# Kernel optimization log

Hardware: AMD Instinct MI355X
Metric: run time of the kernel (lower is better)

## Reference

```python
import jax, jax.numpy as jnp
import numpy as np

H = 16          # num heads
D = 128         # head dim
WIN = 128       # local sliding window
EPS = 1e-6
ROPE_BASE = 500000.0


def rmsnorm(x, w, eps=EPS):
    var = jnp.mean(x * x, axis=-1, keepdims=True)
    return x * jax.lax.rsqrt(var + eps) * w


def rope(x, positions):
    # x: [T, H, D], neox-style rotate-halves
    half = D // 2
    inv_freq = 1.0 / (ROPE_BASE ** (jnp.arange(half, dtype=jnp.float32) / half * 2.0 / 2.0 * 2.0))
    inv_freq = 1.0 / (ROPE_BASE ** (jnp.arange(0, D, 2, dtype=jnp.float32) / D))
    ang = positions.astype(jnp.float32)[:, None] * inv_freq[None, :]      # [T, D/2]
    cos, sin = jnp.cos(ang)[:, None, :], jnp.sin(ang)[:, None, :]         # [T, 1, D/2]
    x1, x2 = x[..., :half], x[..., half:]
    return jnp.concatenate([x1 * cos - x2 * sin, x2 * cos + x1 * sin], axis=-1)


def attend(q, k, v, mask, scale):
    # q,k,v: [T, H, D]; mask: [T, T] (True = attend)
    scores = jnp.einsum('thd,shd->hts', q, k) * scale
    scores = jnp.where(mask[None], scores, jnp.finfo(scores.dtype).min)
    p = jax.nn.softmax(scores, axis=-1)
    return jnp.einsum('hts,shd->thd', p, v)


def setup_inputs() -> dict:
    key = jax.random.key(0)
    ks = jax.random.split(key, 8)
    T, hid = 2048, 2048
    s = 0.02
    return {
        'hidden_states': jax.random.normal(ks[0], (T, hid), jnp.float32),
        'positions': jnp.arange(T, dtype=jnp.int32),
        'Wq': jax.random.normal(ks[1], (hid, H * D + H), jnp.float32) * s,
        'Wk': jax.random.normal(ks[2], (hid, H * D), jnp.float32) * s,
        'Wv': jax.random.normal(ks[3], (hid, H * D), jnp.float32) * s,
        'Wo': jax.random.normal(ks[4], (H * D, hid), jnp.float32) * s,
        'q_norm_w': jnp.ones((hid,), jnp.float32),
        'k_norm_w': jnp.ones((H * D,), jnp.float32),
    }


def reference(hidden_states, positions, Wq, Wk, Wv, Wo, q_norm_w, k_norm_w):
    T = hidden_states.shape[0]
    scale = D ** -0.5
    qg = hidden_states @ Wq                             # [T, H*D + H]
    q, gate = qg[:, :H * D], qg[:, H * D:]              # [T, H*D], [T, H]
    k = hidden_states @ Wk
    v = hidden_states @ Wv
    q = rmsnorm(q, q_norm_w)
    k = rmsnorm(k, k_norm_w)
    q = rope(q.reshape(T, H, D), positions)
    k = rope(k.reshape(T, H, D), positions)
    v = v.reshape(T, H, D)
    # masks
    pi, pj = positions[:, None], positions[None, :]
    causal = pi >= pj
    local = causal & ((pi - pj) < WIN)
    global_out = attend(q, k, v, causal, scale)         # [T, H, D]
    local_out = attend(q, k, v, local, scale)           # [T, H, D]
    gate_hard = (jax.nn.sigmoid(gate) > 0.5).astype(hidden_states.dtype)[:, :, None]
    blended = global_out * gate_hard + local_out * (1.0 - gate_hard)
    return blended.reshape(T, H * D) @ Wo
```

## Files before the change

kernel.cpp:

```cpp
#include <hip/hip_runtime.h>

typedef _Float16 f16;
typedef __attribute__((ext_vector_type(8))) _Float16 half8;
typedef __attribute__((ext_vector_type(4))) _Float16 half4v;
typedef __attribute__((ext_vector_type(4))) float floatx4;

#define T_DIM 2048
#define HID   2048
#define NH    16
#define HD    128
#define QG_LD 2064
#define SM_SCALE 0.08838834764831845f
#define NEG_BIG  -1e30f

__device__ __forceinline__ void async16(const void* g, void* l) {
  __builtin_amdgcn_global_load_lds((const __attribute__((address_space(1))) void*)g,
                                   (__attribute__((address_space(3))) void*)l, 16, 0, 0);
}

__global__ __launch_bounds__(256) void transpose_all(const float* __restrict__ Wq,
                                                     const float* __restrict__ Wk,
                                                     const float* __restrict__ Wv,
                                                     f16* __restrict__ WqT, f16* __restrict__ WkT,
                                                     f16* __restrict__ WvT) {
  __shared__ float tile[32][33];
  const int z = blockIdx.z;
  const float* src = (z == 0) ? Wq : ((z == 1) ? Wk : Wv);
  const int ld = (z == 0) ? QG_LD : 2048;
  f16* dst = (z == 0) ? WqT : ((z == 1) ? WkT : WvT);
  const int bx = blockIdx.x * 32, by = blockIdx.y * 32;
  const int tx = threadIdx.x, ty = threadIdx.y;
#pragma unroll
  for (int i = 0; i < 4; ++i)
    tile[ty + 8 * i][tx] = src[(size_t)(by + ty + 8 * i) * ld + bx + tx];
  __syncthreads();
#pragma unroll
  for (int i = 0; i < 4; ++i)
    dst[(size_t)(bx + ty + 8 * i) * HID + by + tx] = (f16)tile[tx][ty + 8 * i];
}

__global__ __launch_bounds__(256) void transpose_w(const float* __restrict__ src, int src_ld,
                                                   f16* __restrict__ dst) {
  __shared__ float tile[32][33];
  const int bx = blockIdx.x * 32, by = blockIdx.y * 32;
  const int tx = threadIdx.x, ty = threadIdx.y;
#pragma unroll
  for (int i = 0; i < 4; ++i)
    tile[ty + 8 * i][tx] = src[(size_t)(by + ty + 8 * i) * src_ld + bx + tx];
  __syncthreads();
#pragma unroll
  for (int i = 0; i < 4; ++i)
    dst[(size_t)(bx + ty + 8 * i) * HID + by + tx] = (f16)tile[tx][ty + 8 * i];
}

__global__ __launch_bounds__(256) void transpose_h(const f16* __restrict__ src, f16* __restrict__ dst) {
  __shared__ f16 tile[32][33];
  const int bx = blockIdx.x * 32, by = blockIdx.y * 32;
  const int tx = threadIdx.x, ty = threadIdx.y;
#pragma unroll
  for (int i = 0; i < 4; ++i)
    tile[ty + 8 * i][tx] = src[(size_t)(by + ty + 8 * i) * T_DIM + bx + tx];
  __syncthreads();
#pragma unroll
  for (int i = 0; i < 4; ++i)
    dst[(size_t)(bx + ty + 8 * i) * T_DIM + by + tx] = tile[tx][ty + 8 * i];
}

__global__ __launch_bounds__(256) void convert_f32_f16(const float* __restrict__ src, f16* __restrict__ dst) {
  const int i = (blockIdx.x * 256 + threadIdx.x) * 4;
  const float4 v = *(const float4*)(src + i);
  half4v o;
  o.x = (f16)v.x; o.y = (f16)v.y; o.z = (f16)v.z; o.w = (f16)v.w;
  *(half4v*)(dst + i) = o;
}

__global__ __launch_bounds__(256) void gate_kernel(const float* __restrict__ hidden,
                                                   const float* __restrict__ Wq,
                                                   float* __restrict__ gate) {
  __shared__ double red[256][16];
  const int t = blockIdx.x, tid = threadIdx.x;
  double sums[16];
#pragma unroll
  for (int h2 = 0; h2 < 16; ++h2) sums[h2] = 0.0;
  const float* hrow = hidden + (size_t)t * HID;
  for (int k = tid; k < HID; k += 256) {
    const double hv = (double)hrow[k];
    const float* wr = Wq + (size_t)k * QG_LD + 2048;
#pragma unroll
    for (int h2 = 0; h2 < 16; ++h2) sums[h2] += hv * (double)wr[h2];
  }
#pragma unroll
  for (int h2 = 0; h2 < 16; ++h2) red[tid][h2] = sums[h2];
  __syncthreads();
  for (int st = 128; st > 0; st >>= 1) {
    if (tid < st) {
#pragma unroll
      for (int h2 = 0; h2 < 16; ++h2) red[tid][h2] += red[tid + st][h2];
    }
    __syncthreads();
  }
  if (tid < 16) gate[(size_t)t * 16 + tid] = (red[0][tid] > 0.0) ? 1.f : 0.f;
}

__global__ __launch_bounds__(256) void norm_rope2(const f16* __restrict__ qsrc, const f16* __restrict__ ksrc,
                                                  const float* __restrict__ qw, const float* __restrict__ kw,
                                                  const int* __restrict__ pos,
                                                  f16* __restrict__ qdst, f16* __restrict__ kdst) {
  __shared__ float row[2048];
  __shared__ float red[256];
  const int t = blockIdx.x & 2047, sel = blockIdx.x >> 11, tid = threadIdx.x;
  const f16* s = (sel ? ksrc : qsrc) + (size_t)t * HID;
  const float* w = sel ? kw : qw;
  f16* dst = sel ? kdst : qdst;
  float ss = 0.f;
#pragma unroll
  for (int e = 0; e < 8; ++e) {
    float v = (float)s[tid + 256 * e];
    row[tid + 256 * e] = v;
    ss += v * v;
  }
  red[tid] = ss;
  __syncthreads();
  for (int st = 128; st > 0; st >>= 1) {
    if (tid < st) red[tid] += red[tid + st];
    __syncthreads();
  }
  const float scl = rsqrtf(red[0] * (1.f / 2048.f) + 1e-6f);
  const float p = (float)pos[t];
#pragma unroll
  for (int e = 0; e < 8; ++e) {
    const int idx = tid + 256 * e;
    const int d = idx & 127;
    const int dh = d & 63;
    const int pidx = (d < 64) ? idx + 64 : idx - 64;
    const float xn = row[idx] * scl * w[idx];
    const float xp = row[pidx] * scl * w[pidx];
    const float inv = __expf(-(float)dh * 0.20503692772194388f);
    float cs, sn;
    sincosf(p * inv, &sn, &cs);
    const float o = (d < 64) ? (xn * cs - xp * sn) : (xn * cs + xp * sn);
    dst[(size_t)t * HID + idx] = (f16)o;
  }
}

__device__ __forceinline__ void gemm_issue(const f16* __restrict__ A, const f16* __restrict__ Bt,
                                           char* As, char* Bs, int m0, int n0, int k0,
                                           int wave, int srow, int scol) {
#pragma unroll
  for (int i = 0; i < 4; ++i) {
    async16(A + (size_t)(m0 + 32 * i + srow) * 2048 + k0 + scol, As + 4096 * i + 1024 * wave);
    async16(Bt + (size_t)(n0 + 32 * i + srow) * 2048 + k0 + scol, Bs + 4096 * i + 1024 * wave);
  }
}

__device__ __forceinline__ void gemm_core_db(const f16* __restrict__ A, const f16* __restrict__ Bt,
                                             f16* As, f16* Bs, floatx4 (&acc)[4][4],
                                             int kbase, int klen) {
  const int tid = threadIdx.x;
  const int lane = tid & 63, wave = tid >> 6;
  const int m0 = blockIdx.y * 128, n0 = blockIdx.x * 128;
  const int mo = (wave >> 1) * 64, no = (wave & 1) * 64;
  const int cn = lane & 15, q16 = lane >> 4;
  const int srow = 8 * wave + (lane >> 3);
  const int scol = (lane & 7) * 8;
  gemm_issue(A, Bt, (char*)As, (char*)Bs, m0, n0, kbase, wave, srow, scol);
  int cur = 0;
  for (int k0 = kbase; k0 < kbase + klen; k0 += 64) {
    __syncthreads();
    if (k0 + 64 < kbase + klen)
      gemm_issue(A, Bt, (char*)(As + (cur ^ 1) * 8192), (char*)(Bs + (cur ^ 1) * 8192),
                 m0, n0, k0 + 64, wave, srow, scol);
    const f16* as = As + cur * 8192;
    const f16* bs = Bs + cur * 8192;
#pragma unroll
    for (int kk = 0; kk < 64; kk += 32) {
      half8 av[4], bv[4];
#pragma unroll
      for (int i = 0; i < 4; ++i) av[i] = *(const half8*)&as[(mo + i * 16 + cn) * 64 + kk + q16 * 8];
#pragma unroll
      for (int i = 0; i < 4; ++i) bv[i] = *(const half8*)&bs[(no + i * 16 + cn) * 64 + kk + q16 * 8];
#pragma unroll
      for (int i = 0; i < 4; ++i)
#pragma unroll
        for (int j = 0; j < 4; ++j)
          acc[i][j] = __builtin_amdgcn_mfma_f32_16x16x32_f16(av[i], bv[j], acc[i][j], 0, 0, 0);
    }
    cur ^= 1;
  }
}

#define NKT 32

__device__ __forceinline__ void stage_half(const f16* __restrict__ src, int row0, int kcol,
                                           char* dst, int wv, int lane) {
  const int rsw = lane >> 3;
  const int csw = ((lane & 7) ^ rsw) << 3;
#pragma unroll
  for (int L = 0; L < 2; ++L)
    async16(src + (size_t)(row0 + L * 64 + wv * 8 + rsw) * 2048 + kcol + csw,
            dst + (L * 64 + wv * 8) * 128);
}

template <int MQ>
__device__ __forceinline__ void ld_a4(half8 (&a)[4][2], const f16* As, int wm, int cn, int q16) {
#pragma unroll
  for (int rf = 0; rf < 4; ++rf)
#pragma unroll
    for (int kh = 0; kh < 2; ++kh) {
      const int R = wm * 128 + MQ * 64 + rf * 16 + cn;
      a[rf][kh] = *(const half8*)&As[R * 64 + (((kh * 4 + q16) ^ (cn & 7)) << 3)];
    }
}

template <int NQ>
__device__ __forceinline__ void ld_b2(half8 (&b)[2][2], const f16* Bs, int wn, int cn, int q16) {
#pragma unroll
  for (int cf = 0; cf < 2; ++cf)
#pragma unroll
    for (int kh = 0; kh < 2; ++kh) {
      const int S = wn * 64 + NQ * 32 + cf * 16 + cn;
      b[cf][kh] = *(const half8*)&Bs[S * 64 + (((kh * 4 + q16) ^ (cn & 7)) << 3)];
    }
}

template <int MQ, int NQ>
__device__ __forceinline__ void mma16(floatx4 (&acc)[8][4], const half8 (&a)[4][2], const half8 (&b)[2][2]) {
#pragma unroll
  for (int kh = 0; kh < 2; ++kh)
#pragma unroll
    for (int rf = 0; rf < 4; ++rf)
#pragma unroll
      for (int cf = 0; cf < 2; ++cf)
        acc[MQ * 4 + rf][NQ * 2 + cf] = __builtin_amdgcn_mfma_f32_16x16x32_f16(
            a[rf][kh], b[cf][kh], acc[MQ * 4 + rf][NQ * 2 + cf], 0, 0, 0);
}

#define LGKM0() asm volatile("s_waitcnt lgkmcnt(0)" ::: "memory")
#define BAR()   __builtin_amdgcn_s_barrier()
#define PRIO(x) __builtin_amdgcn_s_setprio(x)
#define HBASE(p, isB, h) ((char*)lds + (p) * 65536 + (isB) * 32768 + (h) * 16384)

__global__ __launch_bounds__(512, 2) void gemm_qkv8(const f16* __restrict__ A,
                                                    const f16* __restrict__ B0_, const f16* __restrict__ B1_,
                                                    const f16* __restrict__ B2_,
                                                    f16* __restrict__ C0, f16* __restrict__ C1,
                                                    f16* __restrict__ C2) {
  __shared__ __align__(16) f16 lds[65536];
  const int tid = threadIdx.x;
  const int lane = tid & 63, wv = tid >> 6;
  const int wm = wv >> 2, wn = wv & 3;
  const int q16 = lane >> 4, cn = lane & 15;
  const int z = blockIdx.z;
  const f16* Bt = (z == 0) ? B0_ : ((z == 1) ? B1_ : B2_);
  f16* C = (z == 0) ? C0 : ((z == 1) ? C1 : C2);
  const int m0 = blockIdx.y * 256, n0 = blockIdx.x * 256;

  floatx4 acc[8][4] = {};
  half8 a[4][2], b0[2][2], b1[2][2];

  stage_half(A,  m0,       0,  HBASE(0, 0, 0), wv, lane);
  stage_half(Bt, n0,       0,  HBASE(0, 1, 0), wv, lane);
  stage_half(Bt, n0 + 128, 0,  HBASE(0, 1, 1), wv, lane);
  stage_half(A,  m0 + 128, 0,  HBASE(0, 0, 1), wv, lane);
  stage_half(Bt, n0,       64, HBASE(1, 1, 0), wv, lane);
  stage_half(A,  m0,       64, HBASE(1, 0, 0), wv, lane);
  asm volatile("s_waitcnt vmcnt(4)" ::: "memory");
  BAR();

  for (int t = 0; t < NKT; ++t) {
    const int pb = t & 1;
    const f16* As = lds + pb * 32768;
    const f16* Bs = As + 16384;
    ld_a4<0>(a, As, wm, cn, q16);
    ld_b2<0>(b0, Bs, wn, cn, q16);
    if (t + 1 < NKT) stage_half(Bt, n0 + 128, (t + 1) * 64, HBASE(pb ^ 1, 1, 1), wv, lane);
    LGKM0(); BAR();
    PRIO(1); mma16<0, 0>(acc, a, b0); PRIO(0);
    BAR();
    ld_b2<1>(b1, Bs, wn, cn, q16);
    if (t + 1 < NKT) stage_half(A, m0 + 128, (t + 1) * 64, HBASE(pb ^ 1, 0, 1), wv, lane);
    LGKM0(); BAR();
    PRIO(1); mma16<0, 1>(acc, a, b1); PRIO(0);
    BAR();
    ld_a4<1>(a, As, wm, cn, q16);
    if (t + 2 < NKT) stage_half(Bt, n0, (t + 2) * 64, HBASE(pb, 1, 0), wv, lane);
    LGKM0(); BAR();
    PRIO(1); mma16<1, 0>(acc, a, b0); PRIO(0);
    BAR();
    if (t + 2 < NKT) {
      stage_half(A, m0, (t + 2) * 64, HBASE(pb, 0, 0), wv, lane);
      asm volatile("s_waitcnt vmcnt(4)" ::: "memory");
    } else if (t == NKT - 2) {
      asm volatile("s_waitcnt vmcnt(0)" ::: "memory");
    }
    BAR();
    PRIO(1); mma16<1, 1>(acc, a, b1); PRIO(0);
    BAR();
  }

  const int r0 = q16 * 4;
#pragma unroll
  for (int i = 0; i < 8; ++i)
#pragma unroll
    for (int j = 0; j < 4; ++j)
#pragma unroll
      for (int r = 0; r < 4; ++r)
        C[(size_t)(m0 + wm * 128 + i * 16 + r0 + r) * 2048 + n0 + wn * 64 + j * 16 + cn] =
            (f16)acc[i][j][r];
}

__global__ __launch_bounds__(256, 2) void gemm_out_sk(const f16* __restrict__ A, const f16* __restrict__ Bt,
                                                      float* __restrict__ P0, float* __restrict__ P1) {
  __shared__ __align__(16) f16 As[2 * 128 * 64];
  __shared__ __align__(16) f16 Bs[2 * 128 * 64];
  const int z = blockIdx.z;
  floatx4 acc[4][4] = {};
  gemm_core_db(A, Bt, As, Bs, acc, z * 1024, 1024);
  float* C = z ? P1 : P0;
  const int lane = threadIdx.x & 63, wave = threadIdx.x >> 6;
  const int mb = blockIdx.y * 128 + (wave >> 1) * 64;
  const int nb = blockIdx.x * 128 + (wave & 1) * 64;
  const int r0 = (lane >> 4) * 4, cn = lane & 15;
#pragma unroll
  for (int i = 0; i < 4; ++i)
#pragma unroll
    for (int j = 0; j < 4; ++j)
#pragma unroll
      for (int r = 0; r < 4; ++r)
        C[(size_t)(mb + i * 16 + r0 + r) * 2048 + nb + j * 16 + cn] = acc[i][j][r];
}

__global__ __launch_bounds__(256) void add_out(const float* __restrict__ P0, const float* __restrict__ P1,
                                               float* __restrict__ out) {
  const int i = (blockIdx.x * 256 + threadIdx.x) * 4;
  const float4 a = *(const float4*)(P0 + i);
  const float4 b = *(const float4*)(P1 + i);
  float4 o;
  o.x = a.x + b.x; o.y = a.y + b.y; o.z = a.z + b.z; o.w = a.w + b.w;
  *(float4*)(out + i) = o;
}

__global__ __launch_bounds__(256, 2) void flash_kernel(const f16* __restrict__ Qg, const f16* __restrict__ Kg,
                                                       const f16* __restrict__ VTg, const float* __restrict__ gate,
                                                       f16* __restrict__ Oa, float* __restrict__ Opart,
                                                       float2* __restrict__ ml) {
  __shared__ __align__(16) f16 Ks[2][64 * 128];
  __shared__ __align__(16) f16 VTs[2][128 * 64];
  __shared__ __align__(16) f16 Ps[4][16][72];

  const int tid = threadIdx.x;
  const int lane = tid & 63, wv = tid >> 6;
  const int q16 = lane >> 4, cn = lane & 15;
  const int r0 = q16 * 4;

  const int p = blockIdx.x;
  const int o = p >> 4;
  const int h = p & 15;
  int qt, nsp, piece, slot_o;
  if (o < 24)      { qt = 31 - o / 3;        nsp = 3; piece = o % 3;        slot_o = o; }
  else if (o < 36) { qt = 35 - o;            nsp = 1; piece = 0;            slot_o = 0; }
  else             { int u = o - 36; qt = 23 - (u >> 1); nsp = 2; piece = u & 1; slot_o = 24 + u; }
  const int L = qt + 1;
  const int base = L / nsp, rem = L % nsp;
  const int kb = piece * base + (piece < rem ? piece : rem);
  const int ke = kb + base + (piece < rem ? 1 : 0) - 1;
  const bool split = (nsp > 1);
  const int slot = h * 48 + slot_o;
  const int t0 = qt * 64;

  bool gbit[4];
#pragma unroll
  for (int r = 0; r < 4; ++r)
    gbit[r] = gate[(size_t)(t0 + wv * 16 + r0 + r) * NH + h] > 0.5f;

  half8 qa[4];
#pragma unroll
  for (int i = 0; i < 4; ++i)
    qa[i] = *(const half8*)(Qg + (size_t)(t0 + 16 * wv + cn) * HID + h * HD + 32 * i + q16 * 8);

  {
    const int sb = kb * 64;
#pragma unroll
    for (int i = 0; i < 4; ++i) {
      const int rk = 16 * i + 4 * wv + q16;
      async16(Kg + (size_t)(sb + rk) * HID + h * HD + ((cn ^ (rk & 7)) << 3),
              (char*)Ks[0] + 4096 * i + 1024 * wv);
      const int rv = 32 * i + 8 * wv + (lane >> 3);
      async16(VTg + (size_t)(h * HD + rv) * T_DIM + sb + (((lane & 7) ^ (lane >> 3)) << 3),
              (char*)VTs[0] + 4096 * i + 1024 * wv);
    }
  }

  floatx4 og[8] = {};
  floatx4 lacc = {0.f, 0.f, 0.f, 0.f};
  float mg[4];
#pragma unroll
  for (int r = 0; r < 4; ++r) mg[r] = NEG_BIG;

  const half8 ones = {(f16)1, (f16)1, (f16)1, (f16)1, (f16)1, (f16)1, (f16)1, (f16)1};

  int cur = 0;
  for (int kt = kb; kt <= ke; ++kt) {
    const int s0 = kt * 64;
    __syncthreads();
    if (kt < ke) {
      const int sn = s0 + 64;
#pragma unroll
      for (int i = 0; i < 4; ++i) {
        const int rk = 16 * i + 4 * wv + q16;
        async16(Kg + (size_t)(sn + rk) * HID + h * HD + ((cn ^ (rk & 7)) << 3),
                (char*)Ks[cur ^ 1] + 4096 * i + 1024 * wv);
        const int rv = 32 * i + 8 * wv + (lane >> 3);
        async16(VTg + (size_t)(h * HD + rv) * T_DIM + sn + (((lane & 7) ^ (lane >> 3)) << 3),
                (char*)VTs[cur ^ 1] + 4096 * i + 1024 * wv);
      }
    }

    floatx4 sacc[4] = {};
    PRIO(1);
#pragma unroll
    for (int i = 0; i < 4; ++i)
// ... 78 lines not shown
      }
  } else {
    float* ob = Opart + ((size_t)slot * 64 + wv * 16) * 128;
#pragma unroll
    for (int dt = 0; dt < 8; ++dt)
#pragma unroll
      for (int r = 0; r < 4; ++r)
        ob[(r0 + r) * 128 + dt * 16 + cn] = og[dt][r];
    if (cn == 0) {
      float2* mlp = ml + slot * 64 + wv * 16;
#pragma unroll
      for (int r = 0; r < 4; ++r) mlp[r0 + r] = float2{mg[r], lacc[r]};
    }
  }
}

__global__ __launch_bounds__(256) void merge_chunks(const float* __restrict__ Opart,
                                                    const float2* __restrict__ ml,
                                                    f16* __restrict__ attn) {
  const int b = blockIdx.x;
  const int h = b & 15, v = b >> 4;
  const int qt = 12 + v;
  const int n = (qt >= 24) ? 3 : 2;
  const int s0 = (qt >= 24) ? (h * 48 + 3 * (31 - qt)) : (h * 48 + 24 + 2 * (23 - qt));
  const int tid = threadIdx.x;
  const int row = tid >> 2;
  const int cq = (tid & 3) * 32;

  float m = NEG_BIG, mv[3], lv[3];
#pragma unroll
  for (int c = 0; c < 3; ++c) {
    if (c < n) {
      const float2 x = ml[(s0 + c) * 64 + row];
      mv[c] = x.x; lv[c] = x.y;
      m = fmaxf(m, x.x);
    }
  }
  float e[3], denom = 0.f;
#pragma unroll
  for (int c = 0; c < 3; ++c) {
    if (c < n) {
      e[c] = __expf(mv[c] - m);
      denom += e[c] * lv[c];
    }
  }
  const float inv = 1.f / denom;
  f16* out = attn + (size_t)(qt * 64 + row) * 2048 + h * 128 + cq;
#pragma unroll
  for (int i = 0; i < 32; i += 4) {
    float4 acc = {0.f, 0.f, 0.f, 0.f};
#pragma unroll
    for (int c = 0; c < 3; ++c) {
      if (c < n) {
        const float4 a = *(const float4*)(Opart + ((size_t)(s0 + c) * 64 + row) * 128 + cq + i);
        acc.x += e[c] * a.x; acc.y += e[c] * a.y; acc.z += e[c] * a.z; acc.w += e[c] * a.w;
      }
    }
    out[i + 0] = (f16)(acc.x * inv);
    out[i + 1] = (f16)(acc.y * inv);
    out[i + 2] = (f16)(acc.z * inv);
    out[i + 3] = (f16)(acc.w * inv);
  }
}

extern "C" void kernel_launch(void* const* d_in, const int* in_sizes, int n_in,
                              void* d_out, int out_size, void* d_ws, size_t ws_size,
                              hipStream_t stream) {
  const float* hidden = (const float*)d_in[0];
  const int* pos = (const int*)d_in[1];
  const float* Wq = (const float*)d_in[2];
  const float* Wk = (const float*)d_in[3];
  const float* Wv = (const float*)d_in[4];
  const float* Wo = (const float*)d_in[5];
  const float* qw = (const float*)d_in[6];
  const float* kw = (const float*)d_in[7];

  char* ws = (char*)d_ws;
  const size_t MB = 1ull << 20;
  f16* WqT = (f16*)(ws + 0 * MB);
  f16* WkT = (f16*)(ws + 8 * MB);
  f16* WvT = (f16*)(ws + 16 * MB);
  f16* hidh = (f16*)(ws + 24 * MB);
  f16* q_raw = (f16*)(ws + 32 * MB);
  f16* k_raw = (f16*)(ws + 48 * MB);
  f16* v_h = (f16*)(ws + 64 * MB);
  f16* q_h = (f16*)(ws + 72 * MB);
  f16* k_h = (f16*)(ws + 80 * MB);
  float* gate = (float*)(ws + 88 * MB);
  f16* WoT = WqT;
  f16* attn = q_raw;
  f16* vT = k_raw;
  float* P0 = (float*)(ws + 8 * MB);
  float* P1 = (float*)(ws + 72 * MB);
  float* Opart = (float*)(ws + 8 * MB);
  float2* mlbuf = (float2*)(ws + 40 * MB);

  dim3 tb(32, 8);
  transpose_all<<<dim3(64, 64, 3), tb, 0, stream>>>(Wq, Wk, Wv, WqT, WkT, WvT);
  convert_f32_f16<<<4096, 256, 0, stream>>>(hidden, hidh);
  gate_kernel<<<2048, 256, 0, stream>>>(hidden, Wq, gate);
  gemm_qkv8<<<dim3(8, 8, 3), 512, 0, stream>>>(hidh, WqT, WkT, WvT, q_raw, k_raw, v_h);
  transpose_w<<<dim3(64, 64), tb, 0, stream>>>(Wo, 2048, WoT);
  norm_rope2<<<4096, 256, 0, stream>>>(q_raw, k_raw, qw, kw, pos, q_h, k_h);
  transpose_h<<<dim3(64, 64), tb, 0, stream>>>(v_h, vT);
  flash_kernel<<<960, 256, 0, stream>>>(q_h, k_h, vT, gate, attn, Opart, mlbuf);
  merge_chunks<<<320, 256, 0, stream>>>(Opart, mlbuf, attn);
  gemm_out_sk<<<dim3(16, 16, 2), 256, 0, stream>>>(attn, WoT, P0, P1);
  add_out<<<4096, 256, 0, stream>>>(P0, P1, (float*)d_out);
}
```

Before: 348.7 us.

## Fuse QKV GEMM into 256x192 tiles and use 4-way split-K 256x256 output GEMM

The three separate QKV projections become one GEMM over a contiguous transposed weight buffer, using 256x192 tiles (256 blocks instead of 192) with a new staging and pipelining schedule. Outputs are routed by column to the q/k/v buffers, which now sit contiguously in the workspace. The output projection switches from a 128x128 two-way split-K kernel to the 256x256 pipelined kernel with four-way split-K, followed by a four-input reduction. Costs are an extra fp32 partial write and read, and an odd 48-column-per-wave B tile that may be less efficient.

```diff
diff --git a/kernel.cpp b/kernel.cpp
--- a/kernel.cpp
+++ b/kernel.cpp
@@ -143,53 +143,9 @@
   }
 }
 
-__device__ __forceinline__ void gemm_issue(const f16* __restrict__ A, const f16* __restrict__ Bt,
-                                           char* As, char* Bs, int m0, int n0, int k0,
-                                           int wave, int srow, int scol) {
-#pragma unroll
-  for (int i = 0; i < 4; ++i) {
-    async16(A + (size_t)(m0 + 32 * i + srow) * 2048 + k0 + scol, As + 4096 * i + 1024 * wave);
-    async16(Bt + (size_t)(n0 + 32 * i + srow) * 2048 + k0 + scol, Bs + 4096 * i + 1024 * wave);
-  }
-}
-
-__device__ __forceinline__ void gemm_core_db(const f16* __restrict__ A, const f16* __restrict__ Bt,
-                                             f16* As, f16* Bs, floatx4 (&acc)[4][4],
-                                             int kbase, int klen) {
-  const int tid = threadIdx.x;
-  const int lane = tid & 63, wave = tid >> 6;
-  const int m0 = blockIdx.y * 128, n0 = blockIdx.x * 128;
-  const int mo = (wave >> 1) * 64, no = (wave & 1) * 64;
-  const int cn = lane & 15, q16 = lane >> 4;
-  const int srow = 8 * wave + (lane >> 3);
-  const int scol = (lane & 7) * 8;
-  gemm_issue(A, Bt, (char*)As, (char*)Bs, m0, n0, kbase, wave, srow, scol);
-  int cur = 0;
-  for (int k0 = kbase; k0 < kbase + klen; k0 += 64) {
-    __syncthreads();
-    if (k0 + 64 < kbase + klen)
-      gemm_issue(A, Bt, (char*)(As + (cur ^ 1) * 8192), (char*)(Bs + (cur ^ 1) * 8192),
-                 m0, n0, k0 + 64, wave, srow, scol);
-    const f16* as = As + cur * 8192;
-    const f16* bs = Bs + cur * 8192;
-#pragma unroll
-    for (int kk = 0; kk < 64; kk += 32) {
-      half8 av[4], bv[4];
-#pragma unroll
-      for (int i = 0; i < 4; ++i) av[i] = *(const half8*)&as[(mo + i * 16 + cn) * 64 + kk + q16 * 8];
-#pragma unroll
-      for (int i = 0; i < 4; ++i) bv[i] = *(const half8*)&bs[(no + i * 16 + cn) * 64 + kk + q16 * 8];
-#pragma unroll
-      for (int i = 0; i < 4; ++i)
-#pragma unroll
-        for (int j = 0; j < 4; ++j)
-          acc[i][j] = __builtin_amdgcn_mfma_f32_16x16x32_f16(av[i], bv[j], acc[i][j], 0, 0, 0);
-    }
-    cur ^= 1;
-  }
-}
-
-#define NKT 32
+#define LGKM0() asm volatile("s_waitcnt lgkmcnt(0)" ::: "memory")
+#define BAR()   __builtin_amdgcn_s_barrier()
+#define PRIO(x) __builtin_amdgcn_s_setprio(x)
 
 __device__ __forceinline__ void stage_half(const f16* __restrict__ src, int row0, int kcol,
                                            char* dst, int wv, int lane) {
@@ -235,62 +191,167 @@
             a[rf][kh], b[cf][kh], acc[MQ * 4 + rf][NQ * 2 + cf], 0, 0, 0);
 }
 
-#define LGKM0() asm volatile("s_waitcnt lgkmcnt(0)" ::: "memory")
-#define BAR()   __builtin_amdgcn_s_barrier()
-#define PRIO(x) __builtin_amdgcn_s_setprio(x)
 #define HBASE(p, isB, h) ((char*)lds + (p) * 65536 + (isB) * 32768 + (h) * 16384)
 
-__global__ __launch_bounds__(512, 2) void gemm_qkv8(const f16* __restrict__ A,
-                                                    const f16* __restrict__ B0_, const f16* __restrict__ B1_,
-                                                    const f16* __restrict__ B2_,
-                                                    f16* __restrict__ C0, f16* __restrict__ C1,
-                                                    f16* __restrict__ C2) {
+#define NKT 32
+
+__device__ __forceinline__ void stage_piece(const f16* __restrict__ src, int row0, int kcol,
+                                            char* dst, int wv, int lane) {
+  const int rsw = lane >> 3;
+  const int csw = ((lane & 7) ^ rsw) << 3;
+  async16(src + (size_t)(row0 + wv * 8 + rsw) * 2048 + kcol + csw, dst + wv * 1024);
+}
+
+template <int MQ, int KH>
+__device__ __forceinline__ void ld_a1(half8 (&a)[4], const f16* As, int wm, int cn, int q16) {
+#pragma unroll
+  for (int rf = 0; rf < 4; ++rf) {
+    const int R = wm * 128 + MQ * 64 + rf * 16 + cn;
+    a[rf] = *(const half8*)&As[R * 64 + (((KH * 4 + q16) ^ (cn & 7)) << 3)];
+  }
+}
+
+template <int KH>
+__device__ __forceinline__ void ld_b3(half8 (&b)[3], const f16* Bs, int wn, int cn, int q16) {
+#pragma unroll
+  for (int cf = 0; cf < 3; ++cf) {
+    const int S = wn * 48 + cf * 16 + cn;
+    b[cf] = *(const half8*)&Bs[S * 64 + (((KH * 4 + q16) ^ (cn & 7)) << 3)];
+  }
+}
+
+template <int MQ>
+__device__ __forceinline__ void mma12(floatx4 (&acc)[8][3], const half8 (&a)[4], const half8 (&b)[3]) {
+#pragma unroll
+  for (int rf = 0; rf < 4; ++rf)
+#pragma unroll
+    for (int cf = 0; cf < 3; ++cf)
+      acc[MQ * 4 + rf][cf] = __builtin_amdgcn_mfma_f32_16x16x32_f16(
+          a[rf], b[cf], acc[MQ * 4 + rf][cf], 0, 0, 0);
+}
+
+#define QKV_A(q, kt, buf) stage_piece(A,  m0 + (q) * 64, (kt) * 64, ldsb + (buf) * 57344 + (q) * 8192, wv, lane)
+#define QKV_B(p, kt, buf) stage_piece(BT, n0 + (p) * 64, (kt) * 64, ldsb + (buf) * 57344 + 32768 + (p) * 8192, wv, lane)
+
+__global__ __launch_bounds__(512, 2) void gemm_qkv192(const f16* __restrict__ A,
+                                                      const f16* __restrict__ BT,
+                                                      f16* __restrict__ Call) {
+  __shared__ __align__(16) f16 lds[57344];
+  char* const ldsb = (char*)lds;
+  const int tid = threadIdx.x;
+  const int lane = tid & 63, wv = tid >> 6;
+  const int wm = wv >> 2, wn = wv & 3;
+  const int q16 = lane >> 4, cn = lane & 15;
+  const int m0 = blockIdx.y * 256, n0 = blockIdx.x * 192;
+
+  floatx4 acc[8][3] = {};
+  half8 a[4], b0[3], b1[3];
+
+  QKV_B(0, 0, 0); QKV_B(1, 0, 0); QKV_B(2, 0, 0); QKV_A(0, 0, 0); QKV_A(2, 0, 0);
+  QKV_A(1, 0, 0); QKV_A(3, 0, 0);
+  QKV_B(0, 1, 1); QKV_B(1, 1, 1); QKV_B(2, 1, 1); QKV_A(0, 1, 1); QKV_A(2, 1, 1);
+  QKV_A(1, 1, 1); QKV_A(3, 1, 1);
+  asm volatile("s_waitcnt vmcnt(7)" ::: "memory");
+  BAR();
+
+  for (int t = 0; t < NKT; ++t) {
+    const int pb = t & 1;
+    const f16* As = lds + pb * 28672;
+    const f16* Bs = As + 16384;
+    ld_b3<0>(b0, Bs, wn, cn, q16);
+    ld_a1<0, 0>(a, As, wm, cn, q16);
+    if (t >= 1 && t + 1 < NKT) QKV_A(1, t + 1, pb ^ 1);
+    asm volatile("s_waitcnt vmcnt(6)" ::: "memory");
+    LGKM0(); BAR();
+    PRIO(1); mma12<0>(acc, a, b0); PRIO(0);
+    BAR();
+    ld_a1<1, 0>(a, As, wm, cn, q16);
+    if (t >= 1 && t + 1 < NKT) QKV_A(3, t + 1, pb ^ 1);
+    LGKM0(); BAR();
+    PRIO(1); mma12<1>(acc, a, b0); PRIO(0);
+    BAR();
+    ld_b3<1>(b1, Bs, wn, cn, q16);
+    ld_a1<0, 1>(a, As, wm, cn, q16);
+    LGKM0(); BAR();
+    PRIO(1); mma12<0>(acc, a, b1); PRIO(0);
+    BAR();
+    ld_a1<1, 1>(a, As, wm, cn, q16);
+    if (t + 2 < NKT) {
+      QKV_B(0, t + 2, pb); QKV_B(1, t + 2, pb); QKV_B(2, t + 2, pb);
+      QKV_A(0, t + 2, pb); QKV_A(2, t + 2, pb);
+      asm volatile("s_waitcnt vmcnt(7)" ::: "memory");
+    } else if (t == NKT - 2) {
+      asm volatile("s_waitcnt vmcnt(0)" ::: "memory");
+    }
+    LGKM0(); BAR();
+    PRIO(1); mma12<1>(acc, a, b1); PRIO(0);
+    BAR();
+  }
+
+  const int r0 = q16 * 4;
+#pragma unroll
+  for (int j = 0; j < 3; ++j) {
+    const int cb = n0 + wn * 48 + j * 16;
+    f16* Cj = Call + ((size_t)(cb >> 11) << 22) + (cb & 2047) + cn;
+#pragma unroll
+    for (int i = 0; i < 8; ++i)
+#pragma unroll
+      for (int r = 0; r < 4; ++r)
+        Cj[(size_t)(m0 + wm * 128 + i * 16 + r0 + r) * 2048] = (f16)acc[i][j][r];
+  }
+}
+
+#define OKT 8
+
+__global__ __launch_bounds__(512, 2) void gemm_out8(const f16* __restrict__ A, const f16* __restrict__ Bt,
+                                                    float* __restrict__ P0, float* __restrict__ P1,
+                                                    float* __restrict__ P2, float* __restrict__ P3) {
   __shared__ __align__(16) f16 lds[65536];
   const int tid = threadIdx.x;
   const int lane = tid & 63, wv = tid >> 6;
   const int wm = wv >> 2, wn = wv & 3;
   const int q16 = lane >> 4, cn = lane & 15;
   const int z = blockIdx.z;
-  const f16* Bt = (z == 0) ? B0_ : ((z == 1) ? B1_ : B2_);
-  f16* C = (z == 0) ? C0 : ((z == 1) ? C1 : C2);
+  const int kbase = z * 512;
+  float* P = (z == 0) ? P0 : ((z == 1) ? P1 : ((z == 2) ? P2 : P3));
   const int m0 = blockIdx.y * 256, n0 = blockIdx.x * 256;
 
   floatx4 acc[8][4] = {};
   half8 a[4][2], b0[2][2], b1[2][2];
 
-  stage_half(A,  m0,       0,  HBASE(0, 0, 0), wv, lane);
-  stage_half(Bt, n0,       0,  HBASE(0, 1, 0), wv, lane);
-  stage_half(Bt, n0 + 128, 0,  HBASE(0, 1, 1), wv, lane);
-  stage_half(A,  m0 + 128, 0,  HBASE(0, 0, 1), wv, lane);
-  stage_half(Bt, n0,       64, HBASE(1, 1, 0), wv, lane);
-  stage_half(A,  m0,       64, HBASE(1, 0, 0), wv, lane);
+  stage_half(A,  m0,       kbase,      HBASE(0, 0, 0), wv, lane);
+  stage_half(Bt, n0,       kbase,      HBASE(0, 1, 0), wv, lane);
+  stage_half(Bt, n0 + 128, kbase,      HBASE(0, 1, 1), wv, lane);
+  stage_half(A,  m0 + 128, kbase,      HBASE(0, 0, 1), wv, lane);
+  stage_half(Bt, n0,       kbase + 64, HBASE(1, 1, 0), wv, lane);
+  stage_half(A,  m0,       kbase + 64, HBASE(1, 0, 0), wv, lane);
   asm volatile("s_waitcnt vmcnt(4)" ::: "memory");
   BAR();
 
-  for (int t = 0; t < NKT; ++t) {
+  for (int t = 0; t < OKT; ++t) {
     const int pb = t & 1;
     const f16* As = lds + pb * 32768;
     const f16* Bs = As + 16384;
     ld_a4<0>(a, As, wm, cn, q16);
     ld_b2<0>(b0, Bs, wn, cn, q16);
-    if (t + 1 < NKT) stage_half(Bt, n0 + 128, (t + 1) * 64, HBASE(pb ^ 1, 1, 1), wv, lane);
+    if (t + 1 < OKT) stage_half(Bt, n0 + 128, kbase + (t + 1) * 64, HBASE(pb ^ 1, 1, 1), wv, lane);
     LGKM0(); BAR();
     PRIO(1); mma16<0, 0>(acc, a, b0); PRIO(0);
     BAR();
     ld_b2<1>(b1, Bs, wn, cn, q16);
-    if (t + 1 < NKT) stage_half(A, m0 + 128, (t + 1) * 64, HBASE(pb ^ 1, 0, 1), wv, lane);
+    if (t + 1 < OKT) stage_half(A, m0 + 128, kbase + (t + 1) * 64, HBASE(pb ^ 1, 0, 1), wv, lane);
     LGKM0(); BAR();
     PRIO(1); mma16<0, 1>(acc, a, b1); PRIO(0);
     BAR();
     ld_a4<1>(a, As, wm, cn, q16);
-    if (t + 2 < NKT) stage_half(Bt, n0, (t + 2) * 64, HBASE(pb, 1, 0), wv, lane);
+    if (t + 2 < OKT) stage_half(Bt, n0, kbase + (t + 2) * 64, HBASE(pb, 1, 0), wv, lane);
     LGKM0(); BAR();
     PRIO(1); mma16<1, 0>(acc, a, b0); PRIO(0);
     BAR();
-    if (t + 2 < NKT) {
-      stage_half(A, m0, (t + 2) * 64, HBASE(pb, 0, 0), wv, lane);
+    if (t + 2 < OKT) {
+      stage_half(A, m0, kbase + (t + 2) * 64, HBASE(pb, 0, 0), wv, lane);
       asm volatile("s_waitcnt vmcnt(4)" ::: "memory");
-    } else if (t == NKT - 2) {
+    } else if (t == OKT - 2) {
       asm volatile("s_waitcnt vmcnt(0)" ::: "memory");
     }
     BAR();
@@ -305,38 +366,23 @@
     for (int j = 0; j < 4; ++j)
 #pragma unroll
       for (int r = 0; r < 4; ++r)
-        C[(size_t)(m0 + wm * 128 + i * 16 + r0 + r) * 2048 + n0 + wn * 64 + j * 16 + cn] =
-            (f16)acc[i][j][r];
-}
-
-__global__ __launch_bounds__(256, 2) void gemm_out_sk(const f16* __restrict__ A, const f16* __restrict__ Bt,
-                                                      float* __restrict__ P0, float* __restrict__ P1) {
-  __shared__ __align__(16) f16 As[2 * 128 * 64];
-  __shared__ __align__(16) f16 Bs[2 * 128 * 64];
-  const int z = blockIdx.z;
-  floatx4 acc[4][4] = {};
-  gemm_core_db(A, Bt, As, Bs, acc, z * 1024, 1024);
-  float* C = z ? P1 : P0;
-  const int lane = threadIdx.x & 63, wave = threadIdx.x >> 6;
-  const int mb = blockIdx.y * 128 + (wave >> 1) * 64;
-  const int nb = blockIdx.x * 128 + (wave & 1) * 64;
-  const int r0 = (lane >> 4) * 4, cn = lane & 15;
-#pragma unroll
-  for (int i = 0; i < 4; ++i)
-#pragma unroll
-    for (int j = 0; j < 4; ++j)
-#pragma unroll
-      for (int r = 0; r < 4; ++r)
-        C[(size_t)(mb + i * 16 + r0 + r) * 2048 + nb + j * 16 + cn] = acc[i][j][r];
-}
-
-__global__ __launch_bounds__(256) void add_out(const float* __restrict__ P0, const float* __restrict__ P1,
-                                               float* __restrict__ out) {
+        P[(size_t)(m0 + wm * 128 + i * 16 + r0 + r) * 2048 + n0 + wn * 64 + j * 16 + cn] =
+            acc[i][j][r];
+}
+
+__global__ __launch_bounds__(256) void add_out4(const float* __restrict__ P0, const float* __restrict__ P1,
+                                                const float* __restrict__ P2, const float* __restrict__ P3,
+                                                float* __restrict__ out) {
   const int i = (blockIdx.x * 256 + threadIdx.x) * 4;
   const float4 a = *(const float4*)(P0 + i);
   const float4 b = *(const float4*)(P1 + i);
+  const float4 c = *(const float4*)(P2 + i);
+  const float4 d = *(const float4*)(P3 + i);
   float4 o;
-  o.x = a.x + b.x; o.y = a.y + b.y; o.z = a.z + b.z; o.w = a.w + b.w;
+  o.x = (a.x + b.x) + (c.x + d.x);
+  o.y = (a.y + b.y) + (c.y + d.y);
+  o.z = (a.z + b.z) + (c.z + d.z);
+  o.w = (a.w + b.w) + (c.w + d.w);
   *(float4*)(out + i) = o;
 }
 
@@ -581,29 +627,33 @@
   f16* WvT = (f16*)(ws + 16 * MB);
   f16* hidh = (f16*)(ws + 24 * MB);
   f16* q_raw = (f16*)(ws + 32 * MB);
-  f16* k_raw = (f16*)(ws + 48 * MB);
-  f16* v_h = (f16*)(ws + 64 * MB);
+  f16* k_raw = (f16*)(ws + 40 * MB);
+  f16* v_h = (f16*)(ws + 48 * MB);
+  f16* vT = (f16*)(ws + 56 * MB);
+  float2* mlbuf = (float2*)(ws + 64 * MB);
   f16* q_h = (f16*)(ws + 72 * MB);
   f16* k_h = (f16*)(ws + 80 * MB);
   float* gate = (float*)(ws + 88 * MB);
   f16* WoT = WqT;
   f16* attn = q_raw;
-  f16* vT = k_raw;
+  const f16* BT_all = WqT;
+  f16* Call = q_raw;
+  float* Opart = (float*)(ws + 8 * MB);
   float* P0 = (float*)(ws + 8 * MB);
-  float* P1 = (float*)(ws + 72 * MB);
-  float* Opart = (float*)(ws + 8 * MB);
-  float2* mlbuf = (float2*)(ws + 40 * MB);
+  float* P1 = (float*)(ws + 40 * MB);
+  float* P2 = (float*)(ws + 56 * MB);
+  float* P3 = (float*)(ws + 72 * MB);
 
   dim3 tb(32, 8);
   transpose_all<<<dim3(64, 64, 3), tb, 0, stream>>>(Wq, Wk, Wv, WqT, WkT, WvT);
   convert_f32_f16<<<4096, 256, 0, stream>>>(hidden, hidh);
   gate_kernel<<<2048, 256, 0, stream>>>(hidden, Wq, gate);
-  gemm_qkv8<<<dim3(8, 8, 3), 512, 0, stream>>>(hidh, WqT, WkT, WvT, q_raw, k_raw, v_h);
+  gemm_qkv192<<<dim3(32, 8), 512, 0, stream>>>(hidh, BT_all, Call);
   transpose_w<<<dim3(64, 64), tb, 0, stream>>>(Wo, 2048, WoT);
   norm_rope2<<<4096, 256, 0, stream>>>(q_raw, k_raw, qw, kw, pos, q_h, k_h);
   transpose_h<<<dim3(64, 64), tb, 0, stream>>>(v_h, vT);
   flash_kernel<<<960, 256, 0, stream>>>(q_h, k_h, vT, gate, attn, Opart, mlbuf);
   merge_chunks<<<320, 256, 0, stream>>>(Opart, mlbuf, attn);
-  gemm_out_sk<<<dim3(16, 16, 2), 256, 0, stream>>>(attn, WoT, P0, P1);
-  add_out<<<4096, 256, 0, stream>>>(P0, P1, (float*)d_out);
-}
+  gemm_out8<<<dim3(8, 8, 4), 512, 0, stream>>>(attn, WoT, P0, P1, P2, P3);
+  add_out4<<<4096, 256, 0, stream>>>(P0, P1, P2, P3, (float*)d_out);
+}
```

Result: slower. 357.7 us (+2.6%).

## Fuse prep kernels, merge QKV GEMM into one 256x192-tiled launch, fuse post-QKV ops

Applied to the files above, without the earlier changes.

Combines the weight transposes (including Wo), the hidden-state conversion and the gate computation into one prep launch. The three QKV GEMMs become a single GEMM over the concatenated transposed weights, with 256x192 tiles and a reworked software pipeline. Norm/RoPE and the V transpose are also merged into one launch. This cuts launch count and tail effects and gives the QKV GEMM a better wave count (256 blocks), at the cost of a more intricate pipeline with hand-tuned vmcnt waits and a workspace layout that must stay contiguous.

```diff
diff --git a/kernel.cpp b/kernel.cpp
--- a/kernel.cpp
+++ b/kernel.cpp
@@ -18,16 +18,58 @@
                                    (__attribute__((address_space(3))) void*)l, 16, 0, 0);
 }
 
-__global__ __launch_bounds__(256) void transpose_all(const float* __restrict__ Wq,
-                                                     const float* __restrict__ Wk,
-                                                     const float* __restrict__ Wv,
-                                                     f16* __restrict__ WqT, f16* __restrict__ WkT,
-                                                     f16* __restrict__ WvT) {
-  __shared__ float tile[32][33];
+__global__ __launch_bounds__(256) void prep_all(const float* __restrict__ Wq,
+                                                const float* __restrict__ Wk,
+                                                const float* __restrict__ Wv,
+                                                const float* __restrict__ Wo,
+                                                const float* __restrict__ hidden,
+                                                f16* __restrict__ WqT, f16* __restrict__ WkT,
+                                                f16* __restrict__ WvT, f16* __restrict__ WoT,
+                                                f16* __restrict__ hidh, float* __restrict__ gate) {
+  __shared__ __align__(16) char smem[32768];
   const int z = blockIdx.z;
-  const float* src = (z == 0) ? Wq : ((z == 1) ? Wk : Wv);
+  if (z == 4) {
+    const int lb = blockIdx.y * 64 + blockIdx.x;
+    const int tid = threadIdx.y * 32 + threadIdx.x;
+    const int i = (lb * 256 + tid) * 4;
+    const float4 v = *(const float4*)(hidden + i);
+    half4v o;
+    o.x = (f16)v.x; o.y = (f16)v.y; o.z = (f16)v.z; o.w = (f16)v.w;
+    *(half4v*)(hidh + i) = o;
+    return;
+  }
+  if (z == 5) {
+    if (blockIdx.y >= 32) return;
+    double (*red)[16] = (double (*)[16])smem;
+    const int t = blockIdx.y * 64 + blockIdx.x;
+    const int tid = threadIdx.y * 32 + threadIdx.x;
+    double sums[16];
+#pragma unroll
+    for (int h2 = 0; h2 < 16; ++h2) sums[h2] = 0.0;
+    const float* hrow = hidden + (size_t)t * HID;
+    for (int k = tid; k < HID; k += 256) {
+      const double hv = (double)hrow[k];
+      const float* wr = Wq + (size_t)k * QG_LD + 2048;
+#pragma unroll
+      for (int h2 = 0; h2 < 16; ++h2) sums[h2] += hv * (double)wr[h2];
+    }
+#pragma unroll
+    for (int h2 = 0; h2 < 16; ++h2) red[tid][h2] = sums[h2];
+    __syncthreads();
+    for (int st = 128; st > 0; st >>= 1) {
+      if (tid < st) {
+#pragma unroll
+        for (int h2 = 0; h2 < 16; ++h2) red[tid][h2] += red[tid + st][h2];
+      }
+      __syncthreads();
+    }
+    if (tid < 16) gate[(size_t)t * 16 + tid] = (red[0][tid] > 0.0) ? 1.f : 0.f;
+    return;
+  }
+  float (*tile)[33] = (float (*)[33])smem;
+  const float* src = (z == 0) ? Wq : ((z == 1) ? Wk : ((z == 2) ? Wv : Wo));
   const int ld = (z == 0) ? QG_LD : 2048;
-  f16* dst = (z == 0) ? WqT : ((z == 1) ? WkT : WvT);
+  f16* dst = (z == 0) ? WqT : ((z == 1) ? WkT : ((z == 2) ? WvT : WoT));
   const int bx = blockIdx.x * 32, by = blockIdx.y * 32;
   const int tx = threadIdx.x, ty = threadIdx.y;
 #pragma unroll
@@ -39,76 +81,31 @@
     dst[(size_t)(bx + ty + 8 * i) * HID + by + tx] = (f16)tile[tx][ty + 8 * i];
 }
 
-__global__ __launch_bounds__(256) void transpose_w(const float* __restrict__ src, int src_ld,
-                                                   f16* __restrict__ dst) {
-  __shared__ float tile[32][33];
-  const int bx = blockIdx.x * 32, by = blockIdx.y * 32;
-  const int tx = threadIdx.x, ty = threadIdx.y;
-#pragma unroll
-  for (int i = 0; i < 4; ++i)
-    tile[ty + 8 * i][tx] = src[(size_t)(by + ty + 8 * i) * src_ld + bx + tx];
-  __syncthreads();
-#pragma unroll
-  for (int i = 0; i < 4; ++i)
-    dst[(size_t)(bx + ty + 8 * i) * HID + by + tx] = (f16)tile[tx][ty + 8 * i];
-}
-
-__global__ __launch_bounds__(256) void transpose_h(const f16* __restrict__ src, f16* __restrict__ dst) {
-  __shared__ f16 tile[32][33];
-  const int bx = blockIdx.x * 32, by = blockIdx.y * 32;
-  const int tx = threadIdx.x, ty = threadIdx.y;
-#pragma unroll
-  for (int i = 0; i < 4; ++i)
-    tile[ty + 8 * i][tx] = src[(size_t)(by + ty + 8 * i) * T_DIM + bx + tx];
-  __syncthreads();
-#pragma unroll
-  for (int i = 0; i < 4; ++i)
-    dst[(size_t)(bx + ty + 8 * i) * T_DIM + by + tx] = tile[tx][ty + 8 * i];
-}
-
-__global__ __launch_bounds__(256) void convert_f32_f16(const float* __restrict__ src, f16* __restrict__ dst) {
-  const int i = (blockIdx.x * 256 + threadIdx.x) * 4;
-  const float4 v = *(const float4*)(src + i);
-  half4v o;
-  o.x = (f16)v.x; o.y = (f16)v.y; o.z = (f16)v.z; o.w = (f16)v.w;
-  *(half4v*)(dst + i) = o;
-}
-
-__global__ __launch_bounds__(256) void gate_kernel(const float* __restrict__ hidden,
-                                                   const float* __restrict__ Wq,
-                                                   float* __restrict__ gate) {
-  __shared__ double red[256][16];
-  const int t = blockIdx.x, tid = threadIdx.x;
-  double sums[16];
-#pragma unroll
-  for (int h2 = 0; h2 < 16; ++h2) sums[h2] = 0.0;
-  const float* hrow = hidden + (size_t)t * HID;
-  for (int k = tid; k < HID; k += 256) {
-    const double hv = (double)hrow[k];
-    const float* wr = Wq + (size_t)k * QG_LD + 2048;
-#pragma unroll
-    for (int h2 = 0; h2 < 16; ++h2) sums[h2] += hv * (double)wr[h2];
-  }
-#pragma unroll
-  for (int h2 = 0; h2 < 16; ++h2) red[tid][h2] = sums[h2];
-  __syncthreads();
-  for (int st = 128; st > 0; st >>= 1) {
-    if (tid < st) {
-#pragma unroll
-      for (int h2 = 0; h2 < 16; ++h2) red[tid][h2] += red[tid + st][h2];
-    }
+__global__ __launch_bounds__(256) void post_qkv(const f16* __restrict__ qsrc, const f16* __restrict__ ksrc,
+                                                const float* __restrict__ qw, const float* __restrict__ kw,
+                                                const int* __restrict__ pos,
+                                                f16* __restrict__ qdst, f16* __restrict__ kdst,
+                                                const f16* __restrict__ vsrc, f16* __restrict__ vdst) {
+  __shared__ __align__(16) char smem[9216];
+  const int b = blockIdx.x;
+  const int tid = threadIdx.x;
+  if (b >= 4096) {
+    f16 (*tile)[33] = (f16 (*)[33])smem;
+    const int u = b - 4096;
+    const int bx = (u & 63) * 32, by = (u >> 6) * 32;
+    const int tx = tid & 31, ty = tid >> 5;
+#pragma unroll
+    for (int i = 0; i < 4; ++i)
+      tile[ty + 8 * i][tx] = vsrc[(size_t)(by + ty + 8 * i) * T_DIM + bx + tx];
     __syncthreads();
-  }
-  if (tid < 16) gate[(size_t)t * 16 + tid] = (red[0][tid] > 0.0) ? 1.f : 0.f;
-}
-
-__global__ __launch_bounds__(256) void norm_rope2(const f16* __restrict__ qsrc, const f16* __restrict__ ksrc,
-                                                  const float* __restrict__ qw, const float* __restrict__ kw,
-                                                  const int* __restrict__ pos,
-                                                  f16* __restrict__ qdst, f16* __restrict__ kdst) {
-  __shared__ float row[2048];
-  __shared__ float red[256];
-  const int t = blockIdx.x & 2047, sel = blockIdx.x >> 11, tid = threadIdx.x;
+#pragma unroll
+    for (int i = 0; i < 4; ++i)
+      vdst[(size_t)(bx + ty + 8 * i) * T_DIM + by + tx] = tile[tx][ty + 8 * i];
+    return;
+  }
+  float* row = (float*)smem;
+  float* red = (float*)(smem + 8192);
+  const int t = b & 2047, sel = b >> 11;
   const f16* s = (sel ? ksrc : qsrc) + (size_t)t * HID;
   const float* w = sel ? kw : qw;
   f16* dst = sel ? kdst : qdst;
@@ -142,6 +139,10 @@
     dst[(size_t)t * HID + idx] = (f16)o;
   }
 }
+
+#define LGKM0() asm volatile("s_waitcnt lgkmcnt(0)" ::: "memory")
+#define BAR()   __builtin_amdgcn_s_barrier()
+#define PRIO(x) __builtin_amdgcn_s_setprio(x)
 
 __device__ __forceinline__ void gemm_issue(const f16* __restrict__ A, const f16* __restrict__ Bt,
                                            char* As, char* Bs, int m0, int n0, int k0,
@@ -191,122 +192,110 @@
 
 #define NKT 32
 
-__device__ __forceinline__ void stage_half(const f16* __restrict__ src, int row0, int kcol,
-                                           char* dst, int wv, int lane) {
+__device__ __forceinline__ void stage_piece(const f16* __restrict__ src, int row0, int kcol,
+                                            char* dst, int wv, int lane) {
   const int rsw = lane >> 3;
   const int csw = ((lane & 7) ^ rsw) << 3;
-#pragma unroll
-  for (int L = 0; L < 2; ++L)
-    async16(src + (size_t)(row0 + L * 64 + wv * 8 + rsw) * 2048 + kcol + csw,
-            dst + (L * 64 + wv * 8) * 128);
+  async16(src + (size_t)(row0 + wv * 8 + rsw) * 2048 + kcol + csw, dst + wv * 1024);
+}
+
+template <int MQ, int KH>
+__device__ __forceinline__ void ld_a1(half8 (&a)[4], const f16* As, int wm, int cn, int q16) {
+#pragma unroll
+  for (int rf = 0; rf < 4; ++rf) {
+    const int R = wm * 128 + MQ * 64 + rf * 16 + cn;
+    a[rf] = *(const half8*)&As[R * 64 + (((KH * 4 + q16) ^ (cn & 7)) << 3)];
+  }
+}
+
+template <int KH>
+__device__ __forceinline__ void ld_b3(half8 (&b)[3], const f16* Bs, int wn, int cn, int q16) {
+#pragma unroll
+  for (int cf = 0; cf < 3; ++cf) {
+    const int S = wn * 48 + cf * 16 + cn;
+    b[cf] = *(const half8*)&Bs[S * 64 + (((KH * 4 + q16) ^ (cn & 7)) << 3)];
+  }
 }
 
 template <int MQ>
-__device__ __forceinline__ void ld_a4(half8 (&a)[4][2], const f16* As, int wm, int cn, int q16) {
+__device__ __forceinline__ void mma12(floatx4 (&acc)[8][3], const half8 (&a)[4], const half8 (&b)[3]) {
 #pragma unroll
   for (int rf = 0; rf < 4; ++rf)
 #pragma unroll
-    for (int kh = 0; kh < 2; ++kh) {
-      const int R = wm * 128 + MQ * 64 + rf * 16 + cn;
-      a[rf][kh] = *(const half8*)&As[R * 64 + (((kh * 4 + q16) ^ (cn & 7)) << 3)];
-    }
-}
-
-template <int NQ>
-__device__ __forceinline__ void ld_b2(half8 (&b)[2][2], const f16* Bs, int wn, int cn, int q16) {
-#pragma unroll
-  for (int cf = 0; cf < 2; ++cf)
-#pragma unroll
-    for (int kh = 0; kh < 2; ++kh) {
-      const int S = wn * 64 + NQ * 32 + cf * 16 + cn;
-      b[cf][kh] = *(const half8*)&Bs[S * 64 + (((kh * 4 + q16) ^ (cn & 7)) << 3)];
-    }
-}
-
-template <int MQ, int NQ>
-__device__ __forceinline__ void mma16(floatx4 (&acc)[8][4], const half8 (&a)[4][2], const half8 (&b)[2][2]) {
-#pragma unroll
-  for (int kh = 0; kh < 2; ++kh)
-#pragma unroll
-    for (int rf = 0; rf < 4; ++rf)
-#pragma unroll
-      for (int cf = 0; cf < 2; ++cf)
-        acc[MQ * 4 + rf][NQ * 2 + cf] = __builtin_amdgcn_mfma_f32_16x16x32_f16(
-            a[rf][kh], b[cf][kh], acc[MQ * 4 + rf][NQ * 2 + cf], 0, 0, 0);
-}
-
-#define LGKM0() asm volatile("s_waitcnt lgkmcnt(0)" ::: "memory")
-#define BAR()   __builtin_amdgcn_s_barrier()
-#define PRIO(x) __builtin_amdgcn_s_setprio(x)
-#define HBASE(p, isB, h) ((char*)lds + (p) * 65536 + (isB) * 32768 + (h) * 16384)
-
-__global__ __launch_bounds__(512, 2) void gemm_qkv8(const f16* __restrict__ A,
-                                                    const f16* __restrict__ B0_, const f16* __restrict__ B1_,
-                                                    const f16* __restrict__ B2_,
-                                                    f16* __restrict__ C0, f16* __restrict__ C1,
-                                                    f16* __restrict__ C2) {
-  __shared__ __align__(16) f16 lds[65536];
+    for (int cf = 0; cf < 3; ++cf)
+      acc[MQ * 4 + rf][cf] = __builtin_amdgcn_mfma_f32_16x16x32_f16(
+          a[rf], b[cf], acc[MQ * 4 + rf][cf], 0, 0, 0);
+}
+
+#define QKV_A(q, kt, buf) stage_piece(A,  m0 + (q) * 64, (kt) * 64, ldsb + (buf) * 57344 + (q) * 8192, wv, lane)
+#define QKV_B(p, kt, buf) stage_piece(BT, n0 + (p) * 64, (kt) * 64, ldsb + (buf) * 57344 + 32768 + (p) * 8192, wv, lane)
+
+__global__ __launch_bounds__(512, 2) void gemm_qkv192(const f16* __restrict__ A,
+                                                      const f16* __restrict__ BT,
+                                                      f16* __restrict__ Call) {
+  __shared__ __align__(16) f16 lds[57344];
+  char* const ldsb = (char*)lds;
   const int tid = threadIdx.x;
   const int lane = tid & 63, wv = tid >> 6;
   const int wm = wv >> 2, wn = wv & 3;
   const int q16 = lane >> 4, cn = lane & 15;
-  const int z = blockIdx.z;
-  const f16* Bt = (z == 0) ? B0_ : ((z == 1) ? B1_ : B2_);
-  f16* C = (z == 0) ? C0 : ((z == 1) ? C1 : C2);
-  const int m0 = blockIdx.y * 256, n0 = blockIdx.x * 256;
-
-  floatx4 acc[8][4] = {};
-  half8 a[4][2], b0[2][2], b1[2][2];
-
-  stage_half(A,  m0,       0,  HBASE(0, 0, 0), wv, lane);
-  stage_half(Bt, n0,       0,  HBASE(0, 1, 0), wv, lane);
-  stage_half(Bt, n0 + 128, 0,  HBASE(0, 1, 1), wv, lane);
-  stage_half(A,  m0 + 128, 0,  HBASE(0, 0, 1), wv, lane);
-  stage_half(Bt, n0,       64, HBASE(1, 1, 0), wv, lane);
-  stage_half(A,  m0,       64, HBASE(1, 0, 0), wv, lane);
-  asm volatile("s_waitcnt vmcnt(4)" ::: "memory");
+  const int m0 = blockIdx.y * 256, n0 = blockIdx.x * 192;
+
+  floatx4 acc[8][3] = {};
+  half8 a[4], b0[3], b1[3];
+
+  QKV_B(0, 0, 0); QKV_B(1, 0, 0); QKV_B(2, 0, 0); QKV_A(0, 0, 0); QKV_A(2, 0, 0);
+  QKV_A(1, 0, 0); QKV_A(3, 0, 0);
+  QKV_B(0, 1, 1); QKV_B(1, 1, 1); QKV_B(2, 1, 1); QKV_A(0, 1, 1); QKV_A(2, 1, 1);
+  QKV_A(1, 1, 1); QKV_A(3, 1, 1);
+  asm volatile("s_waitcnt vmcnt(7)" ::: "memory");
   BAR();
 
   for (int t = 0; t < NKT; ++t) {
     const int pb = t & 1;
-    const f16* As = lds + pb * 32768;
+    const f16* As = lds + pb * 28672;
     const f16* Bs = As + 16384;
-    ld_a4<0>(a, As, wm, cn, q16);
-    ld_b2<0>(b0, Bs, wn, cn, q16);
-    if (t + 1 < NKT) stage_half(Bt, n0 + 128, (t + 1) * 64, HBASE(pb ^ 1, 1, 1), wv, lane);
-    LGKM0(); BAR();
-    PRIO(1); mma16<0, 0>(acc, a, b0); PRIO(0);
+    ld_b3<0>(b0, Bs, wn, cn, q16);
+    ld_a1<0, 0>(a, As, wm, cn, q16);
+    if (t >= 1 && t + 1 < NKT) QKV_A(1, t + 1, pb ^ 1);
+    asm volatile("s_waitcnt vmcnt(6)" ::: "memory");
+    BAR(); LGKM0();
+    PRIO(1); mma12<0>(acc, a, b0); PRIO(0);
     BAR();
-    ld_b2<1>(b1, Bs, wn, cn, q16);
-    if (t + 1 < NKT) stage_half(A, m0 + 128, (t + 1) * 64, HBASE(pb ^ 1, 0, 1), wv, lane);
-    LGKM0(); BAR();
-    PRIO(1); mma16<0, 1>(acc, a, b1); PRIO(0);
+    ld_a1<1, 0>(a, As, wm, cn, q16);
+    if (t >= 1 && t + 1 < NKT) QKV_A(3, t + 1, pb ^ 1);
+    BAR(); LGKM0();
+    PRIO(1); mma12<1>(acc, a, b0); PRIO(0);
     BAR();
-    ld_a4<1>(a, As, wm, cn, q16);
-    if (t + 2 < NKT) stage_half(Bt, n0, (t + 2) * 64, HBASE(pb, 1, 0), wv, lane);
-    LGKM0(); BAR();
-    PRIO(1); mma16<1, 0>(acc, a, b0); PRIO(0);
+    ld_b3<1>(b1, Bs, wn, cn, q16);
+    ld_a1<0, 1>(a, As, wm, cn, q16);
+    BAR(); LGKM0();
+    PRIO(1); mma12<0>(acc, a, b1); PRIO(0);
     BAR();
+    ld_a1<1, 1>(a, As, wm, cn, q16);
     if (t + 2 < NKT) {
-      stage_half(A, m0, (t + 2) * 64, HBASE(pb, 0, 0), wv, lane);
-      asm volatile("s_waitcnt vmcnt(4)" ::: "memory");
+      QKV_B(0, t + 2, pb); QKV_B(1, t + 2, pb); QKV_B(2, t + 2, pb);
+      QKV_A(0, t + 2, pb); QKV_A(2, t + 2, pb);
+      asm volatile("s_waitcnt vmcnt(7)" ::: "memory");
     } else if (t == NKT - 2) {
       asm volatile("s_waitcnt vmcnt(0)" ::: "memory");
     }
+    BAR(); LGKM0();
+    PRIO(1); mma12<1>(acc, a, b1); PRIO(0);
     BAR();
-    PRIO(1); mma16<1, 1>(acc, a, b1); PRIO(0);
-    BAR();
   }
 
   const int r0 = q16 * 4;
 #pragma unroll
-  for (int i = 0; i < 8; ++i)
-#pragma unroll
-    for (int j = 0; j < 4; ++j)
+  for (int j = 0; j < 3; ++j) {
+    const int cb = n0 + wn * 48 + j * 16;
+    f16* Cj = Call + ((size_t)(cb >> 11) << 22) + (cb & 2047) + cn;
+#pragma unroll
+    for (int i = 0; i < 8; ++i)
 #pragma unroll
       for (int r = 0; r < 4; ++r)
-        C[(size_t)(m0 + wm * 128 + i * 16 + r0 + r) * 2048 + n0 + wn * 64 + j * 16 + cn] =
-            (f16)acc[i][j][r];
+        Cj[(size_t)(m0 + wm * 128 + i * 16 + r0 + r) * 2048] = (f16)acc[i][j][r];
+  }
 }
 
 __global__ __launch_bounds__(256, 2) void gemm_out_sk(const f16* __restrict__ A, const f16* __restrict__ Bt,
@@ -581,27 +570,26 @@
   f16* WvT = (f16*)(ws + 16 * MB);
   f16* hidh = (f16*)(ws + 24 * MB);
   f16* q_raw = (f16*)(ws + 32 * MB);
-  f16* k_raw = (f16*)(ws + 48 * MB);
-  f16* v_h = (f16*)(ws + 64 * MB);
+  f16* k_raw = (f16*)(ws + 40 * MB);
+  f16* v_h = (f16*)(ws + 48 * MB);
+  f16* vT = (f16*)(ws + 56 * MB);
+  f16* WoT = (f16*)(ws + 64 * MB);
   f16* q_h = (f16*)(ws + 72 * MB);
   f16* k_h = (f16*)(ws + 80 * MB);
   float* gate = (float*)(ws + 88 * MB);
-  f16* WoT = WqT;
+  float2* mlbuf = (float2*)(ws + 88 * MB + 131072);
   f16* attn = q_raw;
-  f16* vT = k_raw;
+  const f16* BT_all = WqT;
+  f16* Call = q_raw;
+  float* Opart = (float*)(ws + 8 * MB);
   float* P0 = (float*)(ws + 8 * MB);
-  float* P1 = (float*)(ws + 72 * MB);
-  float* Opart = (float*)(ws + 8 * MB);
-  float2* mlbuf = (float2*)(ws + 40 * MB);
+  float* P1 = (float*)(ws + 40 * MB);
 
   dim3 tb(32, 8);
-  transpose_all<<<dim3(64, 64, 3), tb, 0, stream>>>(Wq, Wk, Wv, WqT, WkT, WvT);
-  convert_f32_f16<<<4096, 256, 0, stream>>>(hidden, hidh);
-  gate_kernel<<<2048, 256, 0, stream>>>(hidden, Wq, gate);
-  gemm_qkv8<<<dim3(8, 8, 3), 512, 0, stream>>>(hidh, WqT, WkT, WvT, q_raw, k_raw, v_h);
-  transpose_w<<<dim3(64, 64), tb, 0, stream>>>(Wo, 2048, WoT);
-  norm_rope2<<<4096, 256, 0, stream>>>(q_raw, k_raw, qw, kw, pos, q_h, k_h);
-  transpose_h<<<dim3(64, 64), tb, 0, stream>>>(v_h, vT);
+  prep_all<<<dim3(64, 64, 6), tb, 0, stream>>>(Wq, Wk, Wv, Wo, hidden,
+                                               WqT, WkT, WvT, WoT, hidh, gate);
+  gemm_qkv192<<<dim3(32, 8), 512, 0, stream>>>(hidh, BT_all, Call);
+  post_qkv<<<8192, 256, 0, stream>>>(q_raw, k_raw, qw, kw, pos, q_h, k_h, v_h, vT);
   flash_kernel<<<960, 256, 0, stream>>>(q_h, k_h, vT, gate, attn, Opart, mlbuf);
   merge_chunks<<<320, 256, 0, stream>>>(Opart, mlbuf, attn);
   gemm_out_sk<<<dim3(16, 16, 2), 256, 0, stream>>>(attn, WoT, P0, P1);
```

New measurement: 335.3 us. 3.9% less time.
